# Kernel optimization log

Measured on AMD Instinct MI355X. Metric: run time of the kernel, lower is better.

## Reference

```python
import jax, jax.numpy as jnp
import numpy as np

N, DIM, E = 50000, 128, 600000


def setup_inputs() -> dict:
    key = jax.random.key(0)
    ks = jax.random.split(key, 10)
    scale = 1.0 / np.sqrt(DIM)
    return {
        "s": jax.random.normal(ks[0], (N, DIM), jnp.float32),
        "v": jax.random.normal(ks[1], (N, 3, DIM), jnp.float32),
        "edge_index": jax.random.randint(ks[2], (2, E), 0, N, jnp.int32),
        # linear_q: Linear(dim, dim); stored as [in, out] so y = x @ W + b
        "Wq": jax.random.normal(ks[3], (DIM, DIM), jnp.float32) * scale,
        "bq": jnp.zeros((DIM,), jnp.float32),
        # linear_kv: Linear(dim, 3*dim)
        "Wkv": jax.random.normal(ks[4], (DIM, 3 * DIM), jnp.float32) * scale,
        "bkv": jnp.zeros((3 * DIM,), jnp.float32),
        # vec_mlp: Linear(dim, dim)
        "Wvec": jax.random.normal(ks[5], (DIM, DIM), jnp.float32) * scale,
        "bvec": jnp.zeros((DIM,), jnp.float32),
    }


def reference(s, v, edge_index, Wq, bq, Wkv, bkv, Wvec, bvec):
    n_nodes = s.shape[0]
    row, col = edge_index[0], edge_index[1]

    q = s @ Wq + bq                                   # [N, dim]
    kv = s @ Wkv + bkv                                # [N, 3*dim]
    k, v_s, v_v = jnp.split(kv, 3, axis=-1)           # each [N, dim]

    # edge attention weight: per-edge dot product of gathered q/k
    w = jnp.sum(q[row] * k[col], axis=-1, keepdims=True)   # [E, 1]

    edge_msg_s = w * v_s[col]                               # [E, dim]
    # [E,1,1] * [E,1,dim] * [E,3,dim] -> [E,3,dim]
    edge_msg_v = w[:, :, None] * v_v[col][:, None, :] * v[col]

    agg_s = jax.ops.segment_sum(edge_msg_s, row, num_segments=n_nodes)  # [N, dim]
    agg_v = jax.ops.segment_sum(edge_msg_v, row, num_segments=n_nodes)  # [N, 3, dim]

    s_out = s + agg_s
    v_out = v + (agg_v @ Wvec + bvec)
    return (s_out, v_out)
```

## Files before the change

### kernel.cpp

```cpp
#include <hip/hip_runtime.h>
#include <hip/hip_bf16.h>

typedef __attribute__((ext_vector_type(8))) __bf16 bf16x8;
typedef __attribute__((ext_vector_type(4))) float f32x4;


__global__ void prep_kernel(const int* __restrict__ row, int* __restrict__ cnt, int e,
                            const float* __restrict__ Wq, const float* __restrict__ Wkv,
                            const float* __restrict__ Wvec, const float* __restrict__ bq,
                            const float* __restrict__ bkv,
                            __bf16* __restrict__ Wt, float* __restrict__ bM,
                            float* __restrict__ m2, float* __restrict__ c0, int nbh) {
  const int bid = blockIdx.x, tid = threadIdx.x;
  if (bid < nbh) {
    int i = bid * 256 + tid;
    if (i < e) atomicAdd(&cnt[row[i]], 1);
  } else if (bid < nbh + 256) {
    int idx = (bid - nbh) * 256 + tid;
    int c = 128 + (idx >> 7), k = idx & 127;
    float w = (c < 512) ? Wkv[k * 384 + (c - 128)] : Wvec[k * 128 + (c - 512)];
    Wt[c * 128 + k] = (__bf16)w;
  } else if (bid < nbh + 256 + 128) {
    __shared__ float wk[128];
    int c = bid - (nbh + 256);
    if (tid < 128) wk[tid] = Wkv[c * 384 + tid];
    __syncthreads();
    if (tid < 128) {
      float acc = 0.f;
      #pragma unroll 8
      for (int j = 0; j < 128; j++) acc += Wq[tid * 128 + j] * wk[j];
      Wt[c * 128 + tid] = (__bf16)acc;
    } else if (tid == 128) {
      float acc = 0.f;
      for (int j = 0; j < 128; j++) acc += bq[j] * wk[j];
      bM[c] = acc;
    }
  } else {
    if (tid < 128) {
      float acc = 0.f;
      for (int j = 0; j < 128; j++) acc += Wq[tid * 128 + j] * bkv[j];
      m2[tid] = acc;
    } else if (tid == 128) {
      float acc = 0.f;
      for (int j = 0; j < 128; j++) acc += bq[j] * bkv[j];
      c0[0] = acc;
    }
  }
}

__global__ __launch_bounds__(1024) void scan1_kernel(const int* __restrict__ cnt, int* __restrict__ off,
                                                     int* __restrict__ bsum, int n) {
  __shared__ int sh[1024];
  int tid = threadIdx.x;
  int i = blockIdx.x * 1024 + tid;
  int v = (i < n) ? cnt[i] : 0;
  sh[tid] = v;
  __syncthreads();
  for (int d = 1; d < 1024; d <<= 1) {
    int t = (tid >= d) ? sh[tid - d] : 0;
    __syncthreads();
    sh[tid] += t;
    __syncthreads();
  }
  if (i < n) off[i] = sh[tid] - v;
  if (tid == 1023) bsum[blockIdx.x] = sh[1023];
}

__global__ __launch_bounds__(1024) void scan3_kernel(const int* __restrict__ bsum, int* __restrict__ off,
                                                     int* __restrict__ cursor, int n, int e) {
  __shared__ int base_sh;
  const int tid = threadIdx.x;
  if (tid < 64) {
    int part = 0;
    for (int b = tid; b < (int)blockIdx.x; b += 64) part += bsum[b];
    #pragma unroll
    for (int m = 32; m >= 1; m >>= 1) part += __shfl_xor(part, m);
    if (tid == 0) base_sh = part;
  }
  __syncthreads();
  const int base = base_sh;
  int i = blockIdx.x * 1024 + tid;
  if (i < n) { int o = off[i] + base; off[i] = o; cursor[i] = o; }
  if (i == 0) off[n] = e;
}


__global__ __launch_bounds__(256) void gemm1_scatter(
    const int* __restrict__ row, const int* __restrict__ col,
    int* __restrict__ cursor, int* __restrict__ scol, int e, int ngemm,
    const float* __restrict__ s, const __bf16* __restrict__ Wtg,
    const float* __restrict__ bM, const float* __restrict__ bkv,
    const float* __restrict__ m2, const float* __restrict__ c0,
    const float* __restrict__ v,
    __bf16* __restrict__ qb, float* __restrict__ beta,
    __bf16* __restrict__ nodebuf, int n)
{
  __shared__ char uB[34816];
  __bf16* sB = (__bf16*)uB;
  float*  sO = (float*)uB;

  const int tid = threadIdx.x;
  if ((int)blockIdx.x >= ngemm) {
    int i = ((int)blockIdx.x - ngemm) * 256 + tid;
    if (i < e) { int r = row[i]; int pos = atomicAdd(&cursor[r], 1); scol[pos] = col[i]; }
    return;
  }

  const int nb1 = (n + 63) >> 6;
  const int y = ((int)blockIdx.x < nb1) ? 0 : 1;
  const int n0 = (y == 0 ? (int)blockIdx.x : (int)blockIdx.x - nb1) * 64;
  const int wave = tid >> 6, lane = tid & 63;
  const int lr = lane & 15, lg = lane >> 4;
  const int arow = n0 + wave * 16 + lr;

  {
    int r2 = tid >> 1, half = tid & 1;
    int brow = (y == 0) ? r2 : 384 + r2;
    const __bf16* src = &Wtg[(size_t)brow * 128 + half * 64];
    #pragma unroll
    for (int i = 0; i < 8; i++)
      *(bf16x8*)&sB[r2 * 136 + half * 64 + i * 8] = *(const bf16x8*)&src[i * 8];
  }

  bf16x8 a[4];
  if (arow < n) {
    #pragma unroll
    for (int ks = 0; ks < 4; ks++) {
      float4 f0 = *(const float4*)&s[(size_t)arow * 128 + ks * 32 + lg * 8];
      float4 f1 = *(const float4*)&s[(size_t)arow * 128 + ks * 32 + lg * 8 + 4];
      bf16x8 pk;
      pk[0] = (__bf16)f0.x; pk[1] = (__bf16)f0.y; pk[2] = (__bf16)f0.z; pk[3] = (__bf16)f0.w;
      pk[4] = (__bf16)f1.x; pk[5] = (__bf16)f1.y; pk[6] = (__bf16)f1.z; pk[7] = (__bf16)f1.w;
      a[ks] = pk;
    }
  } else {
    #pragma unroll
    for (int ks = 0; ks < 4; ks++) a[ks] = bf16x8{0,0,0,0,0,0,0,0};
  }
  __syncthreads();

  f32x4 acc[8];
  #pragma unroll
  for (int cf = 0; cf < 8; cf++) {
    f32x4 c = {0.f, 0.f, 0.f, 0.f};
    #pragma unroll
    for (int ks = 0; ks < 4; ks++) {
      bf16x8 b = *(const bf16x8*)&sB[(cf * 16 + lr) * 136 + ks * 32 + lg * 8];
      c = __builtin_amdgcn_mfma_f32_16x16x32_bf16(a[ks], b, c, 0, 0, 0);
    }
    acc[cf] = c;
  }
  __syncthreads();

  #pragma unroll
  for (int cf = 0; cf < 8; cf++) {
    int cl = cf * 16 + lr;
    #pragma unroll
    for (int r = 0; r < 4; r++)
      sO[(wave * 16 + lg * 4 + r) * 132 + cl] = acc[cf][r];
  }
  __syncthreads();

  const int drow = tid >> 2, dseg = tid & 3;
  const int dgn = n0 + drow;

  if (y == 0) {
    float part = 0.f;
    #pragma unroll
    for (int ks = 0; ks < 4; ks++)
      #pragma unroll
      for (int j = 0; j < 8; j++)
        part += (float)a[ks][j] * m2[ks * 32 + lg * 8 + j];
    part += __shfl_xor(part, 16);
    part += __shfl_xor(part, 32);
    if (lane < 16 && arow < n) beta[arow] = part + c0[0];

    if (dgn < n) {
      #pragma unroll
      for (int i = 0; i < 4; i++) {
        int cc = dseg * 32 + i * 8;
        bf16x8 pk;
        #pragma unroll
        for (int j = 0; j < 8; j++)
          pk[j] = (__bf16)(sO[drow * 132 + cc + j] + bM[cc + j]);
        *(bf16x8*)&qb[(size_t)dgn * 128 + cc] = pk;
      }
    }
  } else {
    if (arow < n) {
      #pragma unroll
      for (int ks = 0; ks < 4; ks++)
        *(bf16x8*)&nodebuf[(size_t)arow * 512 + ks * 32 + lg * 8] = a[ks];
    }
    if (dgn < n) {
      float vv[32];
      #pragma unroll
      for (int j = 0; j < 32; j++)
        vv[j] = sO[drow * 132 + dseg * 32 + j] + bkv[256 + dseg * 32 + j];
      #pragma unroll
      for (int j3 = 0; j3 < 3; j3++) {
        #pragma unroll
        for (int i = 0; i < 4; i++) {
          int cc = dseg * 32 + i * 8;
          float4 va = *(const float4*)&v[((size_t)dgn * 3 + j3) * 128 + cc];
          float4 vb = *(const float4*)&v[((size_t)dgn * 3 + j3) * 128 + cc + 4];
          bf16x8 pk;
          pk[0] = (__bf16)(vv[i*8+0] * va.x); pk[1] = (__bf16)(vv[i*8+1] * va.y);
          pk[2] = (__bf16)(vv[i*8+2] * va.z); pk[3] = (__bf16)(vv[i*8+3] * va.w);
          pk[4] = (__bf16)(vv[i*8+4] * vb.x); pk[5] = (__bf16)(vv[i*8+5] * vb.y);
          pk[6] = (__bf16)(vv[i*8+6] * vb.z); pk[7] = (__bf16)(vv[i*8+7] * vb.w);
          *(bf16x8*)&nodebuf[(size_t)dgn * 512 + 128 + j3 * 128 + cc] = pk;
        }
      }
    }
  }
}


__device__ inline float2 bf2f(unsigned u) {
  float2 r;
  r.x = __uint_as_float((u & 0xffffu) << 16);
  r.y = __uint_as_float(u & 0xffff0000u);
  return r;
}

__device__ __forceinline__ float dpp_add(float x, const int ctrl) {
  int t;
  switch (ctrl) {
    case 0:  t = __builtin_amdgcn_update_dpp(0, __float_as_int(x), 0xB1, 0xF, 0xF, true); break;
    case 1:  t = __builtin_amdgcn_update_dpp(0, __float_as_int(x), 0x4E, 0xF, 0xF, true); break;
    case 2:  t = __builtin_amdgcn_update_dpp(0, __float_as_int(x), 0x141, 0xF, 0xF, true); break;
    default: t = __builtin_amdgcn_update_dpp(0, __float_as_int(x), 0x140, 0xF, 0xF, true); break;
  }
  return x + __int_as_float(t);
}

__device__ __forceinline__ float row16_sum(float x) {
  x = dpp_add(x, 0); x = dpp_add(x, 1); x = dpp_add(x, 2); x = dpp_add(x, 3);
  return x;
}

#define ACCP(arr, vec) do { float2 _t;                                                \
  _t = bf2f(vec.x); arr[0].x = fmaf(d, _t.x, arr[0].x); arr[0].y = fmaf(d, _t.y, arr[0].y); \
  _t = bf2f(vec.y); arr[1].x = fmaf(d, _t.x, arr[1].x); arr[1].y = fmaf(d, _t.y, arr[1].y); \
  _t = bf2f(vec.z); arr[2].x = fmaf(d, _t.x, arr[2].x); arr[2].y = fmaf(d, _t.y, arr[2].y); \
  _t = bf2f(vec.w); arr[3].x = fmaf(d, _t.x, arr[3].x); arr[3].y = fmaf(d, _t.y, arr[3].y); \
} while (0)

__global__ __launch_bounds__(256) void agg_kernel(
    const int* __restrict__ off, const int* __restrict__ scol,
    const __bf16* __restrict__ qb, const float* __restrict__ beta,
    const char* __restrict__ nodebuf,
    __bf16* __restrict__ gb, float* __restrict__ W1,
    __bf16* __restrict__ aggv16, int n)
{
  const int wid = threadIdx.x >> 6;
  const int lane = threadIdx.x & 63;
  const int nid = blockIdx.x * 4 + wid;
  if (nid >= n) return;
  const int slot = lane >> 4;
  const int fl = lane & 15;

  float qf[8];
  {
    uint4 qu = *(const uint4*)&qb[(size_t)nid * 128 + fl * 8];
    float2 t;
    t = bf2f(qu.x); qf[0] = t.x; qf[1] = t.y;
    t = bf2f(qu.y); qf[2] = t.x; qf[3] = t.y;
    t = bf2f(qu.z); qf[4] = t.x; qf[5] = t.y;
    t = bf2f(qu.w); qf[6] = t.x; qf[7] = t.y;
  }
  const float betar = beta[nid];

  float2 g[4], a0[4], a1[4], a2[4];
  float ws = 0.f;
  #pragma unroll
  for (int i = 0; i < 4; i++) {
    g[i] = make_float2(0.f, 0.f); a0[i] = make_float2(0.f, 0.f);
    a1[i] = make_float2(0.f, 0.f); a2[i] = make_float2(0.f, 0.f);
  }

  const int beg = off[nid];
  const int deg = off[nid + 1] - beg;

  for (int chunk = 0; chunk < deg; chunk += 64) {
    const int cc = (deg - chunk < 64) ? (deg - chunk) : 64;
    int myc = (lane < cc) ? scol[beg + chunk + lane] : 0;

    int c0i = __shfl(myc, (slot < cc) ? slot : 0);
    const char* gp = nodebuf + (size_t)c0i * 1024 + fl * 16;
    uint4 sc = *(const uint4*)(gp);
    uint4 p0 = *(const uint4*)(gp + 256);
    uint4 p1 = *(const uint4*)(gp + 512);
    uint4 p2 = *(const uint4*)(gp + 768);

    for (int j = 0; j < cc; j += 4) {
      const bool more = (j + 4 < cc);
      uint4 nsc, np0, np1, np2;
      if (more) {
        int ni = j + 4 + slot;
        int cn = __shfl(myc, (ni < cc) ? ni : 0);
        const char* gn = nodebuf + (size_t)cn * 1024 + fl * 16;
        nsc = *(const uint4*)(gn);
        np0 = *(const uint4*)(gn + 256);
        np1 = *(const uint4*)(gn + 512);
        np2 = *(const uint4*)(gn + 768);
      }

      float2 t0 = bf2f(sc.x), t1 = bf2f(sc.y), t2 = bf2f(sc.z), t3 = bf2f(sc.w);
      float d = 0.f;
      d = fmaf(qf[0], t0.x, d); d = fmaf(qf[1], t0.y, d);
      d = fmaf(qf[2], t1.x, d); d = fmaf(qf[3], t1.y, d);
      d = fmaf(qf[4], t2.x, d); d = fmaf(qf[5], t2.y, d);
      d = fmaf(qf[6], t3.x, d); d = fmaf(qf[7], t3.y, d);
      d = row16_sum(d) + betar;
      if (j + slot >= cc) d = 0.f;

      g[0].x = fmaf(d, t0.x, g[0].x); g[0].y = fmaf(d, t0.y, g[0].y);
      g[1].x = fmaf(d, t1.x, g[1].x); g[1].y = fmaf(d, t1.y, g[1].y);
      g[2].x = fmaf(d, t2.x, g[2].x); g[2].y = fmaf(d, t2.y, g[2].y);
      g[3].x = fmaf(d, t3.x, g[3].x); g[3].y = fmaf(d, t3.y, g[3].y);
      ws += d;
      ACCP(a0, p0); ACCP(a1, p1); ACCP(a2, p2);

      if (more) { sc = nsc; p0 = np0; p1 = np1; p2 = np2; }
    }
  }

  ws += __shfl_xor(ws, 16); ws += __shfl_xor(ws, 32);
  #pragma unroll
  for (int i = 0; i < 4; i++) {
    g[i].x  += __shfl_xor(g[i].x, 16);  g[i].x  += __shfl_xor(g[i].x, 32);
    g[i].y  += __shfl_xor(g[i].y, 16);  g[i].y  += __shfl_xor(g[i].y, 32);
    a0[i].x += __shfl_xor(a0[i].x, 16); a0[i].x += __shfl_xor(a0[i].x, 32);
    a0[i].y += __shfl_xor(a0[i].y, 16); a0[i].y += __shfl_xor(a0[i].y, 32);
    a1[i].x += __shfl_xor(a1[i].x, 16); a1[i].x += __shfl_xor(a1[i].x, 32);
    a1[i].y += __shfl_xor(a1[i].y, 16); a1[i].y += __shfl_xor(a1[i].y, 32);
    a2[i].x += __shfl_xor(a2[i].x, 16); a2[i].x += __shfl_xor(a2[i].x, 32);
    a2[i].y += __shfl_xor(a2[i].y, 16); a2[i].y += __shfl_xor(a2[i].y, 32);
  }

  if (slot == 0) {
    bf16x8 pk;
    pk[0] = (__bf16)g[0].x; pk[1] = (__bf16)g[0].y; pk[2] = (__bf16)g[1].x; pk[3] = (__bf16)g[1].y;
    pk[4] = (__bf16)g[2].x; pk[5] = (__bf16)g[2].y; pk[6] = (__bf16)g[3].x; pk[7] = (__bf16)g[3].y;
    *(bf16x8*)&gb[(size_t)nid * 128 + fl * 8] = pk;
    if (fl == 0) W1[nid] = ws;

    pk[0] = (__bf16)a0[0].x; pk[1] = (__bf16)a0[0].y; pk[2] = (__bf16)a0[1].x; pk[3] = (__bf16)a0[1].y;
    pk[4] = (__bf16)a0[2].x; pk[5] = (__bf16)a0[2].y; pk[6] = (__bf16)a0[3].x; pk[7] = (__bf16)a0[3].y;
    *(bf16x8*)&aggv16[((size_t)nid * 3 + 0) * 128 + fl * 8] = pk;
    pk[0] = (__bf16)a1[0].x; pk[1] = (__bf16)a1[0].y; pk[2] = (__bf16)a1[1].x; pk[3] = (__bf16)a1[1].y;
    pk[4] = (__bf16)a1[2].x; pk[5] = (__bf16)a1[2].y; pk[6] = (__bf16)a1[3].x; pk[7] = (__bf16)a1[3].y;
    *(bf16x8*)&aggv16[((size_t)nid * 3 + 1) * 128 + fl * 8] = pk;
    pk[0] = (__bf16)a2[0].x; pk[1] = (__bf16)a2[0].y; pk[2] = (__bf16)a2[1].x; pk[3] = (__bf16)a2[1].y;
    pk[4] = (__bf16)a2[2].x; pk[5] = (__bf16)a2[2].y; pk[6] = (__bf16)a2[3].x; pk[7] = (__bf16)a2[3].y;
    *(bf16x8*)&aggv16[((size_t)nid * 3 + 2) * 128 + fl * 8] = pk;
  }
}


__global__ __launch_bounds__(256) void gemm23_mfma(
    const __bf16* __restrict__ Wtg, const float* __restrict__ bkv, const float* __restrict__ bvec,
    const float* __restrict__ s, const float* __restrict__ v,
    const __bf16* __restrict__ gb, const float* __restrict__ W1,
    const __bf16* __restrict__ aggv16,
    float* __restrict__ s_out, float* __restrict__ vout, int n, int nb1)
{
  __shared__ char uB[34816];
  __bf16* sB = (__bf16*)uB;
  float*  sO = (float*)uB;

  const int tid = threadIdx.x;
  const bool smode = (int)blockIdx.x < nb1;
  const int r0 = smode ? blockIdx.x * 64 : (blockIdx.x - nb1) * 64;
  const int rows = smode ? n : 3 * n;
  const int wave = tid >> 6, lane = tid & 63;
  const int lr = lane & 15, lg = lane >> 4;
  const int arow = r0 + wave * 16 + lr;

  {
    int r2 = tid >> 1, half = tid & 1;
    int brow = (smode ? 256 : 512) + r2;
    const __bf16* src = &Wtg[(size_t)brow * 128 + half * 64];
    #pragma unroll
    for (int i = 0; i < 8; i++)
      *(bf16x8*)&sB[r2 * 136 + half * 64 + i * 8] = *(const bf16x8*)&src[i * 8];
  }

  const __bf16* Asrc = smode ? gb : aggv16;
  bf16x8 a[4];
  if (arow < rows) {
    #pragma unroll
    for (int ks = 0; ks < 4; ks++)
      a[ks] = *(const bf16x8*)&Asrc[(size_t)arow * 128 + ks * 32 + lg * 8];
  } else {
    #pragma unroll
    for (int ks = 0; ks < 4; ks++) a[ks] = bf16x8{0,0,0,0,0,0,0,0};
  }
  __syncthreads();

  f32x4 acc[8];
  #pragma unroll
  for (int cf = 0; cf < 8; cf++) {
    f32x4 c = {0.f, 0.f, 0.f, 0.f};
    #pragma unroll
    for (int ks = 0; ks < 4; ks++) {
      bf16x8 b = *(const bf16x8*)&sB[(cf * 16 + lr) * 136 + ks * 32 + lg * 8];
      c = __builtin_amdgcn_mfma_f32_16x16x32_bf16(a[ks], b, c, 0, 0, 0);
    }
    acc[cf] = c;
  }
  __syncthreads();

  #pragma unroll
  for (int cf = 0; cf < 8; cf++) {
    int cl = cf * 16 + lr;
    #pragma unroll
    for (int r = 0; r < 4; r++)
      sO[(wave * 16 + lg * 4 + r) * 132 + cl] = acc[cf][r];
  }
  __syncthreads();

  const int drow = tid >> 2, dseg = tid & 3;
  const int dgr = r0 + drow;

  if (dgr < rows) {
    if (smode) {
      const float w1 = W1[dgr];
      #pragma unroll
      for (int i = 0; i < 8; i++) {
        int cc = dseg * 32 + i * 4;
        float4 sa = *(const float4*)&s[(size_t)dgr * 128 + cc];
        float4 o;
        o.x = sO[drow * 132 + cc + 0] + sa.x + w1 * bkv[128 + cc + 0];
        o.y = sO[drow * 132 + cc + 1] + sa.y + w1 * bkv[128 + cc + 1];
        o.z = sO[drow * 132 + cc + 2] + sa.z + w1 * bkv[128 + cc + 2];
        o.w = sO[drow * 132 + cc + 3] + sa.w + w1 * bkv[128 + cc + 3];
        *(float4*)&s_out[(size_t)dgr * 128 + cc] = o;
      }
    } else {
      #pragma unroll
      for (int i = 0; i < 8; i++) {
        int cc = dseg * 32 + i * 4;
        float4 va = *(const float4*)&v[(size_t)dgr * 128 + cc];
        float4 o;
        o.x = sO[drow * 132 + cc + 0] + va.x + bvec[cc + 0];
        o.y = sO[drow * 132 + cc + 1] + va.y + bvec[cc + 1];
        o.z = sO[drow * 132 + cc + 2] + va.z + bvec[cc + 2];
        o.w = sO[drow * 132 + cc + 3] + va.w + bvec[cc + 3];
        *(float4*)&vout[(size_t)dgr * 128 + cc] = o;
      }
    }
  }
}


extern "C" void kernel_launch(void* const* d_in, const int* in_sizes, int n_in,
                              void* d_out, int out_size, void* d_ws, size_t ws_size,
                              hipStream_t stream)
{
  const float* s    = (const float*)d_in[0];
  const float* v    = (const float*)d_in[1];
  const int*   ei   = (const int*)d_in[2];
  const float* Wq   = (const float*)d_in[3];
  const float* bq   = (const float*)d_in[4];
  const float* Wkv  = (const float*)d_in[5];
  const float* bkv  = (const float*)d_in[6];
  const float* Wvec = (const float*)d_in[7];
  const float* bvec = (const float*)d_in[8];

  const int N = in_sizes[0] / 128;
  const int E = in_sizes[2] / 2;
  const int* row = ei;
  const int* col = ei + E;

  char* ws = (char*)d_ws;
  size_t o = 0;
  auto alloc = [&](size_t bytes) -> char* {
    char* p = ws + o;
    o = (o + bytes + 255) & ~(size_t)255;
    return p;
  };
  int* off    = (int*)alloc((size_t)(N + 1) * 4);
  int* cursor = (int*)alloc((size_t)N * 4);
  int* bsum   = (int*)alloc(4096);
  int* scol   = (int*)alloc((size_t)E * 4);
  __bf16* qb      = (__bf16*)alloc((size_t)N * 128 * 2);
  float*  beta    = (float*)alloc((size_t)N * 4);
  float*  W1      = (float*)alloc((size_t)N * 4);
  __bf16* nodebuf = (__bf16*)alloc((size_t)N * 512 * 2);
  __bf16* Wt      = (__bf16*)alloc((size_t)640 * 128 * 2);
  __bf16* aggv16  = (__bf16*)alloc((size_t)N * 384 * 2);
  __bf16* gb      = (__bf16*)alloc((size_t)N * 128 * 2);
  float*  bM      = (float*)alloc(512);
  float*  m2      = (float*)alloc(512);
  float*  c0      = (float*)alloc(256);

  float* s_out = (float*)d_out;
  float* vout  = (float*)d_out + (size_t)N * 128;

  (void)hipMemsetAsync(cursor, 0, (size_t)N * 4, stream);
  int nbh = (E + 255) / 256;
  prep_kernel<<<nbh + 256 + 128 + 1, 256, 0, stream>>>(row, cursor, E, Wq, Wkv, Wvec, bq, bkv,
                                                       Wt, bM, m2, c0, nbh);
  int nb = (N + 1023) / 1024;
  scan1_kernel<<<nb, 1024, 0, stream>>>(cursor, off, bsum, N);
  scan3_kernel<<<nb, 1024, 0, stream>>>(bsum, off, cursor, N, E);

  int nb1 = (N + 63) / 64;
  int ngemm = 2 * nb1;
  int nbs = (E + 255) / 256;
  gemm1_scatter<<<ngemm + nbs, 256, 0, stream>>>(row, col, cursor, scol, E, ngemm,
                                                 s, Wt, bM, bkv, m2, c0, v,
                                                 qb, beta, nodebuf, N);

  agg_kernel<<<(N + 3) / 4, 256, 0, stream>>>(off, scol, qb, beta, (const char*)nodebuf,
                                              gb, W1, aggv16, N);

  int nb2 = (3 * N + 63) / 64;
  gemm23_mfma<<<nb1 + nb2, 256, 0, stream>>>(Wt, bkv, bvec, s, v, gb, W1, aggv16,
                                             s_out, vout, N, nb1);
}
```

Measured before the change: 276.1 us.

## Split aggregation and output GEMM into halves to overlap across kernels

Splits the node set into two halves. The first half is aggregated alone. A fused launch then aggregates the second half while running the output GEMM on the first half, and a final launch does the GEMM for the second half. The goal is to fill idle compute during the tail of the aggregation and to overlap memory-bound gather work with MFMA GEMM work. The cost is an extra kernel launch, and the fused kernel reserves GEMM shared memory in its agg blocks, which may lower their occupancy.

```diff
diff --git a/kernel.cpp b/kernel.cpp
--- a/kernel.cpp
+++ b/kernel.cpp
@@ -247,17 +247,14 @@
   _t = bf2f(vec.w); arr[3].x = fmaf(d, _t.x, arr[3].x); arr[3].y = fmaf(d, _t.y, arr[3].y); \
 } while (0)
 
-__global__ __launch_bounds__(256) void agg_kernel(
+__device__ __forceinline__ void agg_body(
+    int nid, int lane,
     const int* __restrict__ off, const int* __restrict__ scol,
     const __bf16* __restrict__ qb, const float* __restrict__ beta,
     const char* __restrict__ nodebuf,
     __bf16* __restrict__ gb, float* __restrict__ W1,
-    __bf16* __restrict__ aggv16, int n)
-{
-  const int wid = threadIdx.x >> 6;
-  const int lane = threadIdx.x & 63;
-  const int nid = blockIdx.x * 4 + wid;
-  if (nid >= n) return;
+    __bf16* __restrict__ aggv16)
+{
   const int slot = lane >> 4;
   const int fl = lane & 15;
 
@@ -360,21 +357,21 @@
 }
 
 
-__global__ __launch_bounds__(256) void gemm23_mfma(
+__device__ __forceinline__ void gemm23_body(
+    int bid, int tid, char* uB,
     const __bf16* __restrict__ Wtg, const float* __restrict__ bkv, const float* __restrict__ bvec,
     const float* __restrict__ s, const float* __restrict__ v,
     const __bf16* __restrict__ gb, const float* __restrict__ W1,
     const __bf16* __restrict__ aggv16,
-    float* __restrict__ s_out, float* __restrict__ vout, int n, int nb1)
-{
-  __shared__ char uB[34816];
+    float* __restrict__ s_out, float* __restrict__ vout,
+    int r0s, int rls, int r0v, int rlv, int nbs)
+{
   __bf16* sB = (__bf16*)uB;
   float*  sO = (float*)uB;
 
-  const int tid = threadIdx.x;
-  const bool smode = (int)blockIdx.x < nb1;
-  const int r0 = smode ? blockIdx.x * 64 : (blockIdx.x - nb1) * 64;
-  const int rows = smode ? n : 3 * n;
+  const bool smode = bid < nbs;
+  const int r0 = smode ? r0s + bid * 64 : r0v + (bid - nbs) * 64;
+  const int rlim = smode ? rls : rlv;
   const int wave = tid >> 6, lane = tid & 63;
   const int lr = lane & 15, lg = lane >> 4;
   const int arow = r0 + wave * 16 + lr;
@@ -390,7 +387,7 @@
 
   const __bf16* Asrc = smode ? gb : aggv16;
   bf16x8 a[4];
-  if (arow < rows) {
+  if (arow < rlim) {
     #pragma unroll
     for (int ks = 0; ks < 4; ks++)
       a[ks] = *(const bf16x8*)&Asrc[(size_t)arow * 128 + ks * 32 + lg * 8];
@@ -425,7 +422,7 @@
   const int drow = tid >> 2, dseg = tid & 3;
   const int dgr = r0 + drow;
 
-  if (dgr < rows) {
+  if (dgr < rlim) {
     if (smode) {
       const float w1 = W1[dgr];
       #pragma unroll
@@ -453,6 +450,57 @@
       }
     }
   }
+}
+
+
+__global__ __launch_bounds__(256) void agg_kernel(
+    const int* __restrict__ off, const int* __restrict__ scol,
+    const __bf16* __restrict__ qb, const float* __restrict__ beta,
+    const char* __restrict__ nodebuf,
+    __bf16* __restrict__ gb, float* __restrict__ W1,
+    __bf16* __restrict__ aggv16, int nid0, int nidmax)
+{
+  int nid = nid0 + blockIdx.x * 4 + (threadIdx.x >> 6);
+  if (nid >= nidmax) return;
+  agg_body(nid, threadIdx.x & 63, off, scol, qb, beta, nodebuf, gb, W1, aggv16);
+}
+
+__global__ __launch_bounds__(256) void fused_agg_gemm23(
+    const int* __restrict__ off, const int* __restrict__ scol,
+    const __bf16* __restrict__ qb, const float* __restrict__ beta,
+    const char* __restrict__ nodebuf,
+    __bf16* __restrict__ gb, float* __restrict__ W1,
+    __bf16* __restrict__ aggv16,
+    const __bf16* __restrict__ Wtg, const float* __restrict__ bkv, const float* __restrict__ bvec,
+    const float* __restrict__ s, const float* __restrict__ v,
+    float* __restrict__ s_out, float* __restrict__ vout,
+    int naggblk, int nid0, int nidmax,
+    int r0s, int rls, int r0v, int rlv, int nbs)
+{
+  __shared__ char uB[34816];
+  if ((int)blockIdx.x < naggblk) {
+    int nid = nid0 + blockIdx.x * 4 + (threadIdx.x >> 6);
+    if (nid >= nidmax) return;
+    agg_body(nid, threadIdx.x & 63, off, scol, qb, beta, nodebuf, gb, W1, aggv16);
+  } else {
+    gemm23_body((int)blockIdx.x - naggblk, threadIdx.x, uB,
+                Wtg, bkv, bvec, s, v, gb, W1, aggv16, s_out, vout,
+                r0s, rls, r0v, rlv, nbs);
+  }
+}
+
+__global__ __launch_bounds__(256) void gemm23_kernel(
+    const __bf16* __restrict__ Wtg, const float* __restrict__ bkv, const float* __restrict__ bvec,
+    const float* __restrict__ s, const float* __restrict__ v,
+    const __bf16* __restrict__ gb, const float* __restrict__ W1,
+    const __bf16* __restrict__ aggv16,
+    float* __restrict__ s_out, float* __restrict__ vout,
+    int r0s, int rls, int r0v, int rlv, int nbs)
+{
+  __shared__ char uB[34816];
+  gemm23_body((int)blockIdx.x, threadIdx.x, uB,
+              Wtg, bkv, bvec, s, v, gb, W1, aggv16, s_out, vout,
+              r0s, rls, r0v, rlv, nbs);
 }
 
 
@@ -510,15 +558,31 @@
 
   int nb1 = (N + 63) / 64;
   int ngemm = 2 * nb1;
-  int nbs = (E + 255) / 256;
-  gemm1_scatter<<<ngemm + nbs, 256, 0, stream>>>(row, col, cursor, scol, E, ngemm,
-                                                 s, Wt, bM, bkv, m2, c0, v,
-                                                 qb, beta, nodebuf, N);
-
-  agg_kernel<<<(N + 3) / 4, 256, 0, stream>>>(off, scol, qb, beta, (const char*)nodebuf,
-                                              gb, W1, aggv16, N);
-
-  int nb2 = (3 * N + 63) / 64;
-  gemm23_mfma<<<nb1 + nb2, 256, 0, stream>>>(Wt, bkv, bvec, s, v, gb, W1, aggv16,
-                                             s_out, vout, N, nb1);
-}
+  int nbs_sc = (E + 255) / 256;
+  gemm1_scatter<<<ngemm + nbs_sc, 256, 0, stream>>>(row, col, cursor, scol, E, ngemm,
+                                                    s, Wt, bM, bkv, m2, c0, v,
+                                                    qb, beta, nodebuf, N);
+
+  int Nh = ((N / 2 + 63) / 64) * 64;
+  if (Nh > N) Nh = N;
+  int aggb1 = (Nh + 3) / 4;
+  int aggb2 = (N - Nh + 3) / 4;
+
+  agg_kernel<<<aggb1, 256, 0, stream>>>(off, scol, qb, beta, (const char*)nodebuf,
+                                        gb, W1, aggv16, 0, Nh);
+
+  int nbs1 = (Nh + 63) / 64;
+  int nbv1 = (3 * Nh + 63) / 64;
+  fused_agg_gemm23<<<aggb2 + nbs1 + nbv1, 256, 0, stream>>>(
+      off, scol, qb, beta, (const char*)nodebuf, gb, W1, aggv16,
+      Wt, bkv, bvec, s, v, s_out, vout,
+      aggb2, Nh, N,
+      0, Nh, 0, 3 * Nh, nbs1);
+
+  int ns2 = N - Nh;
+  int nbs2 = (ns2 + 63) / 64;
+  int nbv2 = (3 * N - 3 * Nh + 63) / 64;
+  gemm23_kernel<<<nbs2 + nbv2, 256, 0, stream>>>(
+      Wt, bkv, bvec, s, v, gb, W1, aggv16, s_out, vout,
+      Nh, N, 3 * Nh, 3 * N, nbs2);
+}
```

Measured after the change: 288.3 us. 4.4% more time.

## Double GEMM block tile to 128 rows and stage outputs in bf16 shared memory

Applied to the files above, without the earlier changes.

Both MFMA GEMM kernels (gemm1_scatter and gemm23_mfma) now use 512-thread blocks covering 128 rows instead of 64. The shared-memory output staging buffer changes from fp32 to bf16 so the larger tile still fits in the same LDS allocation. The weight-tile load is re-indexed for the larger thread count, and the scatter portion processes 512 edges per block. The aim is to cut per-block overhead and weight reloads. The costs are an extra bf16 rounding of the GEMM results before the bias and residual adds, and a possible register cap from the (512, 8) launch bounds that could cause spills.

```diff
diff --git a/kernel.cpp b/kernel.cpp
--- a/kernel.cpp
+++ b/kernel.cpp
@@ -85,7 +85,7 @@
 }
 
 
-__global__ __launch_bounds__(256) void gemm1_scatter(
+__global__ __launch_bounds__(512, 8) void gemm1_scatter(
     const int* __restrict__ row, const int* __restrict__ col,
     int* __restrict__ cursor, int* __restrict__ scol, int e, int ngemm,
     const float* __restrict__ s, const __bf16* __restrict__ Wtg,
@@ -97,29 +97,28 @@
 {
   __shared__ char uB[34816];
   __bf16* sB = (__bf16*)uB;
-  float*  sO = (float*)uB;
+  __bf16* sO = (__bf16*)uB;
 
   const int tid = threadIdx.x;
   if ((int)blockIdx.x >= ngemm) {
-    int i = ((int)blockIdx.x - ngemm) * 256 + tid;
+    int i = ((int)blockIdx.x - ngemm) * 512 + tid;
     if (i < e) { int r = row[i]; int pos = atomicAdd(&cursor[r], 1); scol[pos] = col[i]; }
     return;
   }
 
-  const int nb1 = (n + 63) >> 6;
+  const int nb1 = (n + 127) >> 7;
   const int y = ((int)blockIdx.x < nb1) ? 0 : 1;
-  const int n0 = (y == 0 ? (int)blockIdx.x : (int)blockIdx.x - nb1) * 64;
+  const int n0 = (y == 0 ? (int)blockIdx.x : (int)blockIdx.x - nb1) * 128;
   const int wave = tid >> 6, lane = tid & 63;
   const int lr = lane & 15, lg = lane >> 4;
   const int arow = n0 + wave * 16 + lr;
 
   {
-    int r2 = tid >> 1, half = tid & 1;
-    int brow = (y == 0) ? r2 : 384 + r2;
-    const __bf16* src = &Wtg[(size_t)brow * 128 + half * 64];
-    #pragma unroll
-    for (int i = 0; i < 8; i++)
-      *(bf16x8*)&sB[r2 * 136 + half * 64 + i * 8] = *(const bf16x8*)&src[i * 8];
+    int r2 = tid >> 2, q = tid & 3;
+    const __bf16* src = &Wtg[(size_t)((y == 0 ? 0 : 384) + r2) * 128 + q * 32];
+    #pragma unroll
+    for (int i = 0; i < 4; i++)
+      *(bf16x8*)&sB[r2 * 136 + q * 32 + i * 8] = *(const bf16x8*)&src[i * 8];
   }
 
   bf16x8 a[4];
@@ -157,7 +156,7 @@
     int cl = cf * 16 + lr;
     #pragma unroll
     for (int r = 0; r < 4; r++)
-      sO[(wave * 16 + lg * 4 + r) * 132 + cl] = acc[cf][r];
+      sO[(wave * 16 + lg * 4 + r) * 136 + cl] = (__bf16)acc[cf][r];
   }
   __syncthreads();
 
@@ -182,7 +181,7 @@
         bf16x8 pk;
         #pragma unroll
         for (int j = 0; j < 8; j++)
-          pk[j] = (__bf16)(sO[drow * 132 + cc + j] + bM[cc + j]);
+          pk[j] = (__bf16)((float)sO[drow * 136 + cc + j] + bM[cc + j]);
         *(bf16x8*)&qb[(size_t)dgn * 128 + cc] = pk;
       }
     }
@@ -196,7 +195,7 @@
       float vv[32];
       #pragma unroll
       for (int j = 0; j < 32; j++)
-        vv[j] = sO[drow * 132 + dseg * 32 + j] + bkv[256 + dseg * 32 + j];
+        vv[j] = (float)sO[drow * 136 + dseg * 32 + j] + bkv[256 + dseg * 32 + j];
       #pragma unroll
       for (int j3 = 0; j3 < 3; j3++) {
         #pragma unroll
@@ -360,7 +359,7 @@
 }
 
 
-__global__ __launch_bounds__(256) void gemm23_mfma(
+__global__ __launch_bounds__(512, 8) void gemm23_mfma(
     const __bf16* __restrict__ Wtg, const float* __restrict__ bkv, const float* __restrict__ bvec,
     const float* __restrict__ s, const float* __restrict__ v,
     const __bf16* __restrict__ gb, const float* __restrict__ W1,
@@ -369,23 +368,22 @@
 {
   __shared__ char uB[34816];
   __bf16* sB = (__bf16*)uB;
-  float*  sO = (float*)uB;
+  __bf16* sO = (__bf16*)uB;
 
   const int tid = threadIdx.x;
   const bool smode = (int)blockIdx.x < nb1;
-  const int r0 = smode ? blockIdx.x * 64 : (blockIdx.x - nb1) * 64;
+  const int r0 = (smode ? (int)blockIdx.x : (int)blockIdx.x - nb1) * 128;
   const int rows = smode ? n : 3 * n;
   const int wave = tid >> 6, lane = tid & 63;
   const int lr = lane & 15, lg = lane >> 4;
   const int arow = r0 + wave * 16 + lr;
 
   {
-    int r2 = tid >> 1, half = tid & 1;
-    int brow = (smode ? 256 : 512) + r2;
-    const __bf16* src = &Wtg[(size_t)brow * 128 + half * 64];
-    #pragma unroll
-    for (int i = 0; i < 8; i++)
-      *(bf16x8*)&sB[r2 * 136 + half * 64 + i * 8] = *(const bf16x8*)&src[i * 8];
+    int r2 = tid >> 2, q = tid & 3;
+    const __bf16* src = &Wtg[(size_t)((smode ? 256 : 512) + r2) * 128 + q * 32];
+    #pragma unroll
+    for (int i = 0; i < 4; i++)
+      *(bf16x8*)&sB[r2 * 136 + q * 32 + i * 8] = *(const bf16x8*)&src[i * 8];
   }
 
   const __bf16* Asrc = smode ? gb : aggv16;
@@ -418,7 +416,7 @@
     int cl = cf * 16 + lr;
     #pragma unroll
     for (int r = 0; r < 4; r++)
-      sO[(wave * 16 + lg * 4 + r) * 132 + cl] = acc[cf][r];
+      sO[(wave * 16 + lg * 4 + r) * 136 + cl] = (__bf16)acc[cf][r];
   }
   __syncthreads();
 
@@ -433,10 +431,10 @@
         int cc = dseg * 32 + i * 4;
         float4 sa = *(const float4*)&s[(size_t)dgr * 128 + cc];
         float4 o;
-        o.x = sO[drow * 132 + cc + 0] + sa.x + w1 * bkv[128 + cc + 0];
-        o.y = sO[drow * 132 + cc + 1] + sa.y + w1 * bkv[128 + cc + 1];
-        o.z = sO[drow * 132 + cc + 2] + sa.z + w1 * bkv[128 + cc + 2];
-        o.w = sO[drow * 132 + cc + 3] + sa.w + w1 * bkv[128 + cc + 3];
+        o.x = (float)sO[drow * 136 + cc + 0] + sa.x + w1 * bkv[128 + cc + 0];
+        o.y = (float)sO[drow * 136 + cc + 1] + sa.y + w1 * bkv[128 + cc + 1];
+        o.z = (float)sO[drow * 136 + cc + 2] + sa.z + w1 * bkv[128 + cc + 2];
+        o.w = (float)sO[drow * 136 + cc + 3] + sa.w + w1 * bkv[128 + cc + 3];
         *(float4*)&s_out[(size_t)dgr * 128 + cc] = o;
       }
     } else {
@@ -445,10 +443,10 @@
         int cc = dseg * 32 + i * 4;
         float4 va = *(const float4*)&v[(size_t)dgr * 128 + cc];
         float4 o;
-        o.x = sO[drow * 132 + cc + 0] + va.x + bvec[cc + 0];
-        o.y = sO[drow * 132 + cc + 1] + va.y + bvec[cc + 1];
-        o.z = sO[drow * 132 + cc + 2] + va.z + bvec[cc + 2];
-        o.w = sO[drow * 132 + cc + 3] + va.w + bvec[cc + 3];
+        o.x = (float)sO[drow * 136 + cc + 0] + va.x + bvec[cc + 0];
+        o.y = (float)sO[drow * 136 + cc + 1] + va.y + bvec[cc + 1];
+        o.z = (float)sO[drow * 136 + cc + 2] + va.z + bvec[cc + 2];
+        o.w = (float)sO[drow * 136 + cc + 3] + va.w + bvec[cc + 3];
         *(float4*)&vout[(size_t)dgr * 128 + cc] = o;
       }
     }
@@ -508,17 +506,18 @@
   scan1_kernel<<<nb, 1024, 0, stream>>>(cursor, off, bsum, N);
   scan3_kernel<<<nb, 1024, 0, stream>>>(bsum, off, cursor, N, E);
 
-  int nb1 = (N + 63) / 64;
-  int ngemm = 2 * nb1;
-  int nbs = (E + 255) / 256;
-  gemm1_scatter<<<ngemm + nbs, 256, 0, stream>>>(row, col, cursor, scol, E, ngemm,
-                                                 s, Wt, bM, bkv, m2, c0, v,
-                                                 qb, beta, nodebuf, N);
+  int nb1g = (N + 127) / 128;
+  int ngemm = 2 * nb1g;
+  int nbs_sc = (E + 511) / 512;
+  gemm1_scatter<<<ngemm + nbs_sc, 512, 0, stream>>>(row, col, cursor, scol, E, ngemm,
+                                                    s, Wt, bM, bkv, m2, c0, v,
+                                                    qb, beta, nodebuf, N);
 
   agg_kernel<<<(N + 3) / 4, 256, 0, stream>>>(off, scol, qb, beta, (const char*)nodebuf,
                                               gb, W1, aggv16, N);
 
-  int nb2 = (3 * N + 63) / 64;
-  gemm23_mfma<<<nb1 + nb2, 256, 0, stream>>>(Wt, bkv, bvec, s, v, gb, W1, aggv16,
-                                             s_out, vout, N, nb1);
-}
+  int nb1o = (N + 127) / 128;
+  int nb2o = (3 * N + 127) / 128;
+  gemm23_mfma<<<nb1o + nb2o, 512, 0, stream>>>(Wt, bkv, bvec, s, v, gb, W1, aggv16,
+                                               s_out, vout, N, nb1o);
+}
```

Result: slower. 314.9 us (+14.1%).
